# Performance work log

Measured on AMD Instinct MI355X. Metric: run time of the kernel, lower is better.

## Reference

```python
import jax, jax.numpy as jnp
import numpy as np

BATCH, SEQ = 2, 1024
D_MODEL, N_LAYER, VOCAB = 1024, 4, 32000
D_STATE, D_CONV, D_INNER, DT_RANK = 16, 4, 2048, 64  # expand=2, dt_rank=d_model//16
EPS = 1e-5


def setup_inputs() -> dict:
    key = jax.random.key(0)
    ks = jax.random.split(key, 8)
    s = 0.02
    tokens = jax.random.randint(ks[0], (BATCH, SEQ), 0, VOCAB)
    embed = jax.random.normal(ks[1], (VOCAB, D_MODEL), jnp.float32) * s
    norm_w = jnp.ones((N_LAYER, D_MODEL), jnp.float32)
    in_proj_w = jax.random.normal(ks[2], (N_LAYER, 2 * D_INNER, D_MODEL), jnp.float32) * s
    conv_w = jax.random.normal(ks[3], (N_LAYER, D_INNER, D_CONV), jnp.float32) * s
    conv_b = jnp.zeros((N_LAYER, D_INNER), jnp.float32)
    x_proj_w = jax.random.normal(ks[4], (N_LAYER, DT_RANK + 2 * D_STATE, D_INNER), jnp.float32) * s
    dt_w = jax.random.normal(ks[5], (N_LAYER, D_INNER, DT_RANK), jnp.float32) * s
    # softplus-inverse of 0.01 so initial dt is small and positive (mamba default style)
    dt_b = jnp.full((N_LAYER, D_INNER), float(np.log(np.expm1(0.01))), jnp.float32)
    # S4D-real init: A_n = n for n = 1..d_state
    A_log = jnp.log(jnp.broadcast_to(jnp.arange(1, D_STATE + 1, dtype=jnp.float32), (N_LAYER, D_INNER, D_STATE)))
    D_skip = jnp.ones((N_LAYER, D_INNER), jnp.float32)
    out_proj_w = jax.random.normal(ks[6], (N_LAYER, D_MODEL, D_INNER), jnp.float32) * s
    final_norm_w = jnp.ones((D_MODEL,), jnp.float32)
    return dict(tokens=tokens, embed=embed, norm_w=norm_w, in_proj_w=in_proj_w,
                conv_w=conv_w, conv_b=conv_b, x_proj_w=x_proj_w, dt_w=dt_w, dt_b=dt_b,
                A_log=A_log, D_skip=D_skip, out_proj_w=out_proj_w, final_norm_w=final_norm_w)


def rmsnorm(x, w):
    return x * jax.lax.rsqrt(jnp.mean(x * x, axis=-1, keepdims=True) + EPS) * w


def mamba_mixer(x, in_w, cw, cb, xp_w, dtw, dtb, A_log, Dsk, ow):
    # x: (B, L, D)
    xz = jnp.einsum('bld,ed->ble', x, in_w)          # (B, L, 2*d_inner)
    xi, z = jnp.split(xz, 2, axis=-1)
    # causal depthwise conv over L
    xt = jnp.pad(jnp.transpose(xi, (0, 2, 1)), ((0, 0), (0, 0), (D_CONV - 1, 0)))  # (B, C, L+pad)
    xc = jax.lax.conv_general_dilated(xt, cw[:, None, :], (1,), 'VALID',
                                      feature_group_count=D_INNER,
                                      dimension_numbers=('NCH', 'OIH', 'NCH'))
    xc = jax.nn.silu(jnp.transpose(xc, (0, 2, 1)) + cb)  # (B, L, C)
    # input-dependent dt, B, C
    x_dbl = jnp.einsum('blc,ec->ble', xc, xp_w)
    dtr = x_dbl[..., :DT_RANK]
    Bm = x_dbl[..., DT_RANK:DT_RANK + D_STATE]
    Cm = x_dbl[..., DT_RANK + D_STATE:]
    dt = jax.nn.softplus(jnp.einsum('blr,cr->blc', dtr, dtw) + dtb)  # (B, L, C)
    A = -jnp.exp(A_log)  # (C, S)

    def step(h, inp):
        dt_t, x_t, B_t, C_t = inp            # (B,C),(B,C),(B,S),(B,S)
        dA = jnp.exp(dt_t[..., None] * A)    # (B, C, S)
        h = dA * h + (dt_t * x_t)[..., None] * B_t[:, None, :]
        y = jnp.einsum('bcs,bs->bc', h, C_t)
        return h, y

    h0 = jnp.zeros((x.shape[0], D_INNER, D_STATE), x.dtype)
    xs = (jnp.moveaxis(dt, 1, 0), jnp.moveaxis(xc, 1, 0),
          jnp.moveaxis(Bm, 1, 0), jnp.moveaxis(Cm, 1, 0))
    _, ys = jax.lax.scan(step, h0, xs)
    y = jnp.moveaxis(ys, 0, 1) + xc * Dsk
    y = y * jax.nn.silu(z)
    return jnp.einsum('blc,dc->bld', y, ow)


def reference(tokens, embed, norm_w, in_proj_w, conv_w, conv_b, x_proj_w, dt_w, dt_b,
              A_log, D_skip, out_proj_w, final_norm_w):
    h = embed[tokens]  # (B, L, D)
    for i in range(N_LAYER):
        h = h + mamba_mixer(rmsnorm(h, norm_w[i]), in_proj_w[i], conv_w[i], conv_b[i],
                            x_proj_w[i], dt_w[i], dt_b[i], A_log[i], D_skip[i], out_proj_w[i])
    h = rmsnorm(h, final_norm_w)
    logits = jnp.einsum('bld,vd->blv', h, embed)  # tied lm_head
    return logits
```

## Files before the change

kernel.cpp:

```cpp
#include <hip/hip_runtime.h>
#include <cstdint>
#include <cstddef>

#define B_  2
#define L_  1024
#define DM  1024
#define DI  2048
#define DSN 16
#define DR  64

typedef short          s16x8 __attribute__((ext_vector_type(8)));
typedef float          f32x4 __attribute__((ext_vector_type(4)));
typedef unsigned short u16;
typedef unsigned short u16x4 __attribute__((ext_vector_type(4)));
typedef unsigned int   u32x4 __attribute__((ext_vector_type(4)));

__device__ __forceinline__ u16 f2bf(float f) {
  union { float f; unsigned int u; } v; v.f = f;
  unsigned int u = v.u;
  u += 0x7fffu + ((u >> 16) & 1u);
  return (u16)(u >> 16);
}

template <int CTRL>
__device__ __forceinline__ float dpp_add(float x) {
  union { float f; int i; } u, r;
  u.f = x;
  r.i = __builtin_amdgcn_update_dpp(0, u.i, CTRL, 0xf, 0xf, false);
  return x + r.f;
}

#define GLDS(gsrc, ldst)                                                      \
  __builtin_amdgcn_global_load_lds(                                           \
      (const __attribute__((address_space(1))) unsigned int*)(gsrc),          \
      (__attribute__((address_space(3))) unsigned int*)(ldst), 16, 0, 0)

__global__ __launch_bounds__(256) void k_cvt_bf16(const float* __restrict__ in,
                                                  u16* __restrict__ out, int n4) {
  int i = blockIdx.x * 256 + threadIdx.x;
  if (i < n4) {
    f32x4 v = *(const f32x4*)(in + (size_t)i * 4);
    u16x4 o;
    o[0] = f2bf(v[0]); o[1] = f2bf(v[1]); o[2] = f2bf(v[2]); o[3] = f2bf(v[3]);
    *(u16x4*)(out + (size_t)i * 4) = o;
  }
}

__global__ __launch_bounds__(256) void k_gather(const int* __restrict__ tok,
                                                const float* __restrict__ emb,
                                                float* __restrict__ h) {
  int row = blockIdx.x;
  int t = tok[row];
  f32x4 v = ((const f32x4*)(emb + (size_t)t * DM))[threadIdx.x];
  ((f32x4*)(h + (size_t)row * DM))[threadIdx.x] = v;
}

__global__ __launch_bounds__(256) void k_rmsnorm_bf16(const float* __restrict__ x,
                                                      const float* __restrict__ w,
                                                      u16* __restrict__ out) {
  int row = blockIdx.x;
  int tid = threadIdx.x;
  f32x4 v = ((const f32x4*)(x + (size_t)row * DM))[tid];
  float ss = v[0]*v[0] + v[1]*v[1] + v[2]*v[2] + v[3]*v[3];
  #pragma unroll
  for (int m = 1; m < 64; m <<= 1) ss += __shfl_xor(ss, m);
  __shared__ float red[4];
  if ((tid & 63) == 0) red[tid >> 6] = ss;
  __syncthreads();
  float tot = red[0] + red[1] + red[2] + red[3];
  float sc = rsqrtf(tot * (1.0f / DM) + 1e-5f);
  f32x4 wv = ((const f32x4*)w)[tid];
  u16x4 o;
  o[0] = f2bf(v[0]*sc*wv[0]); o[1] = f2bf(v[1]*sc*wv[1]);
  o[2] = f2bf(v[2]*sc*wv[2]); o[3] = f2bf(v[3]*sc*wv[3]);
  ((u16x4*)(out + (size_t)row * DM))[tid] = o;
}

__global__ __launch_bounds__(256) void k_conv_silu(const float* __restrict__ xz,
                                                   const float* __restrict__ cw,
                                                   const float* __restrict__ cb,
                                                   float* __restrict__ xcf,
                                                   u16* __restrict__ xcbf) {
  int e = blockIdx.x * 256 + threadIdx.x;
  int c = e & (DI - 1);
  int row = e >> 11;
  int l = row & (L_ - 1);
  const float* base = xz + (size_t)row * (2 * DI) + c;
  float acc = cb[c];
  float w0 = cw[c*4+0], w1 = cw[c*4+1], w2 = cw[c*4+2], w3 = cw[c*4+3];
  if (l >= 3) acc += base[-3 * (2 * DI)] * w0;
  if (l >= 2) acc += base[-2 * (2 * DI)] * w1;
  if (l >= 1) acc += base[-1 * (2 * DI)] * w2;
  acc += base[0] * w3;
  float s = acc / (1.f + __expf(-acc));
  xcf[e] = s;
  xcbf[e] = f2bf(s);
}

__global__ __launch_bounds__(256) void k_scan(const float* __restrict__ dt,
                                              const float* __restrict__ xcf,
                                              const float* __restrict__ xdbl,
                                              const float* __restrict__ xz,
                                              const float* __restrict__ A_log,
                                              const float* __restrict__ Dsk,
                                              u16* __restrict__ ybf) {
  const int b  = blockIdx.x >> 7;
  const int c0 = (blockIdx.x & 127) << 4;
  const int tid = threadIdx.x;
  const int cl = tid >> 4, s = tid & 15;
  const int c  = c0 + cl;
  const float a2  = -__expf(A_log[c * DSN + s]) * 1.4426950408889634f;
  const float dsk = Dsk[c];

  __shared__ __align__(16) float sdt[16][68], sxc[16][68], sB[16][68], sC[16][68];
  __shared__ float szg[64][17];

  float hs = 0.f, ysel = 0.f;
  const size_t rowbase = (size_t)b * L_;

  float gdt[4], gxc[4], gz[4], gB[4], gC[4];
  auto stage_load = [&](int t0) {
    #pragma unroll
    for (int k = 0; k < 4; ++k) {
      size_t r = rowbase + t0 + cl + 16 * k;
      gdt[k] = dt  [r * DI + c0 + s];
      gxc[k] = xcf [r * DI + c0 + s];
      gz[k]  = xz  [r * (2 * DI) + DI + c0 + s];
      gB[k]  = xdbl[r * 96 + 64 + s];
      gC[k]  = xdbl[r * 96 + 80 + s];
    }
  };
  auto stage_write = [&]() {
    #pragma unroll
    for (int k = 0; k < 4; ++k) {
      int tt = cl + 16 * k;
      sdt[s][tt] = gdt[k];
      sxc[s][tt] = gxc[k];
      sB [s][tt] = gB[k];
      sC [s][tt] = gC[k];
      szg[tt][s] = gz[k];
    }
  };

  stage_load(0);
  stage_write();
  __syncthreads();

  for (int t0 = 0; t0 < L_; t0 += 64) {
    const bool more = (t0 + 64) < L_;
    if (more) stage_load(t0 + 64);

    f32x4 vdt = *(const f32x4*)&sdt[cl][0];
    f32x4 vxc = *(const f32x4*)&sxc[cl][0];
    f32x4 vB  = *(const f32x4*)&sB [s][0];
    f32x4 vC  = *(const f32x4*)&sC [s][0];
    #pragma unroll
    for (int q = 0; q < 16; ++q) {
      f32x4 ndt, nxc, nB, nC;
      if (q < 15) {
        ndt = *(const f32x4*)&sdt[cl][q * 4 + 4];
        nxc = *(const f32x4*)&sxc[cl][q * 4 + 4];
        nB  = *(const f32x4*)&sB [s][q * 4 + 4];
        nC  = *(const f32x4*)&sC [s][q * 4 + 4];
      }
      #pragma unroll
      for (int j = 0; j < 4; ++j) {
        float dtvj = vdt[j], xvj = vxc[j];
        float dA = exp2f(dtvj * a2);
        hs = dA * hs + (dtvj * xvj) * vB[j];
        float yv = hs * vC[j];
        yv = dpp_add<0xB1>(yv);
        yv = dpp_add<0x4E>(yv);
        yv = dpp_add<0x141>(yv);
        yv = dpp_add<0x140>(yv);
        yv += xvj * dsk;
        const int sidx = ((q & 3) << 2) | j;
        ysel = (sidx == s) ? yv : ysel;
      }
      if ((q & 3) == 3) {
        int tt = ((q >> 2) << 4) + s;
        float zv = szg[tt][cl];
        float sig = __builtin_amdgcn_rcpf(1.f + __expf(-zv));
        float yo = ysel * (zv * sig);
        ybf[(rowbase + t0 + tt) * DI + c] = f2bf(yo);
      }
      if (q < 15) { vdt = ndt; vxc = nxc; vB = nB; vC = nC; }
    }
    __syncthreads();
    if (more) stage_write();
    __syncthreads();
  }
}

template <int WM, int WN, int EPI>
__global__ __launch_bounds__(256) void k_gemm(const u16* __restrict__ A,
                                              const u16* __restrict__ W,
                                              float* __restrict__ C,
                                              u16* __restrict__ aux,
                                              const float* __restrict__ bias,
                                              int M, int N, int K) {
  constexpr int BM = 32 * WM, BN = 32 * WN, BK = 32;
  __shared__ __align__(16) u16 As[BM * BK];
  __shared__ __align__(16) u16 Bs[BN * BK];
  const int tid = threadIdx.x;

  const int gx = gridDim.x;
  const int nwg = gx * gridDim.y;
  const int lin = blockIdx.y * gx + blockIdx.x;
  const int q8 = nwg >> 3, r8 = nwg & 7;
  const int xcd = lin & 7, loc = lin >> 3;
  const int swz = (xcd < r8 ? xcd * (q8 + 1) : r8 * (q8 + 1) + (xcd - r8) * q8) + loc;
  const int m0 = (swz / gx) * BM, n0 = (swz % gx) * BN;

  const int wave = tid >> 6, lane = tid & 63;
  const int wm = wave & 1, wn = wave >> 1;
  const int l15 = lane & 15, quad = lane >> 4;
  const int sr = lane >> 2, scc = lane & 3;

  f32x4 acc[WM][WN];
  #pragma unroll
  for (int i = 0; i < WM; ++i)
    #pragma unroll
    for (int j = 0; j < WN; ++j)
      acc[i][j] = f32x4{0.f, 0.f, 0.f, 0.f};

  constexpr int NA = BM / 16;
  constexpr int NB = BN / 16;

  for (int k0 = 0; k0 < K; k0 += BK) {
    for (int ch = wave; ch < NA; ch += 4) {
      int r = (ch << 4) + sr;
      GLDS(A + (size_t)(m0 + r) * K + k0 + (scc << 3), As + (ch << 9));
    }
    for (int ch = wave; ch < NB; ch += 4) {
      int r = (ch << 4) + sr;
      GLDS(W + (size_t)(n0 + r) * K + k0 + (scc << 3), Bs + (ch << 9));
    }
    __syncthreads();
    s16x8 af[WM], bfv[WN];
    #pragma unroll
    for (int i = 0; i < WM; ++i)
      af[i] = *(const s16x8*)(As + (wm * WM * 16 + i * 16 + l15) * BK + quad * 8);
    #pragma unroll
    for (int j = 0; j < WN; ++j)
      bfv[j] = *(const s16x8*)(Bs + (wn * WN * 16 + j * 16 + l15) * BK + quad * 8);
    #pragma unroll
    for (int i = 0; i < WM; ++i)
      #pragma unroll
      for (int j = 0; j < WN; ++j)
        acc[i][j] = __builtin_amdgcn_mfma_f32_16x16x32_bf16(af[i], bfv[j], acc[i][j], 0, 0, 0);
    __syncthreads();
  }

  #pragma unroll
  for (int i = 0; i < WM; ++i) {
    #pragma unroll
    for (int j = 0; j < WN; ++j) {
      int mb = m0 + wm * WM * 16 + i * 16 + quad * 4;
      int nb = n0 + wn * WN * 16 + j * 16 + l15;
      #pragma unroll
      for (int r = 0; r < 4; ++r) {
        size_t idx = (size_t)(mb + r) * N + nb;
        float v = acc[i][j][r];
        if constexpr (EPI == 1) v += C[idx];
        if constexpr (EPI == 2) {
          v += bias[nb];
          v = (v > 20.f) ? v : log1pf(__expf(v));
        }
        C[idx] = v;
        if constexpr (EPI == 3) {
          if (nb < DR) aux[(size_t)(mb + r) * DR + nb] = f2bf(v);
        }
      }
    }
  }
}

extern "C" void kernel_launch(void* const* d_in, const int* in_sizes, int n_in,
                              void* d_out, int out_size, void* d_ws, size_t ws_size,
                              hipStream_t stream) {
  const int*   tokens = (const int*)d_in[0];
  const float* embed  = (const float*)d_in[1];
  const float* norm_w = (const float*)d_in[2];
  const float* in_w   = (const float*)d_in[3];
  const float* conv_w = (const float*)d_in[4];
  const float* conv_b = (const float*)d_in[5];
  const float* xp_w   = (const float*)d_in[6];
  const float* dt_w   = (const float*)d_in[7];
  const float* dt_b   = (const float*)d_in[8];
  const float* A_log  = (const float*)d_in[9];
  const float* D_skip = (const float*)d_in[10];
  const float* out_w  = (const float*)d_in[11];
  const float* fnw    = (const float*)d_in[12];
  float* logits = (float*)d_out;

  char* ws = (char*)d_ws;
  size_t off = 0;
  auto alloc = [&](size_t bytes) -> void* {
    void* p = ws + off;
    off = (off + bytes + 255) & ~(size_t)255;
    return p;
  };
  const size_t R = (size_t)B_ * L_;
  float* h     = (float*)alloc(R * DM * 4);
  u16*   xbf   = (u16*)  alloc(R * DM * 2);
  float* xz    = (float*)alloc(R * 2 * DI * 4);
  float* xcf   = (float*)alloc(R * DI * 4);
  u16*   xcbf  = (u16*)  alloc(R * DI * 2);
  float* xdbl  = (float*)alloc(R * 96 * 4);
  u16*   dtrbf = (u16*)  alloc(R * DR * 2);
  float* dtv   = (float*)alloc(R * DI * 4);
  u16*   ybf   = (u16*)  alloc(R * DI * 2);
  u16*   w_in  = (u16*)  alloc((size_t)2 * DI * DM * 2);
  u16*   w_out = (u16*)  alloc((size_t)DM * DI * 2);
  u16*   w_xp  = (u16*)  alloc((size_t)96 * DI * 2);
  u16*   w_dt  = (u16*)  alloc((size_t)DI * DR * 2);
  u16*   embbf = (u16*)  alloc(32000ull * DM * 2);
  if (off > ws_size) return;

  auto cvt = [&](const float* src, u16* dst, size_t n) {
    int n4 = (int)(n / 4);
    k_cvt_bf16<<<(n4 + 255) / 256, 256, 0, stream>>>(src, dst, n4);
  };
  cvt(embed, embbf, 32000ull * DM);

  k_gather<<<(int)R, 256, 0, stream>>>(tokens, embed, h);

  for (int i = 0; i < 4; ++i) {
    cvt(in_w  + (size_t)i * 2 * DI * DM, w_in,  (size_t)2 * DI * DM);
    cvt(out_w + (size_t)i * DM * DI,     w_out, (size_t)DM * DI);
    cvt(xp_w  + (size_t)i * 96 * DI,     w_xp,  (size_t)96 * DI);
    cvt(dt_w  + (size_t)i * DI * DR,     w_dt,  (size_t)DI * DR);

    k_rmsnorm_bf16<<<(int)R, 256, 0, stream>>>(h, norm_w + i * DM, xbf);
    k_gemm<4, 4, 0><<<dim3(2 * DI / 128, (int)R / 128), 256, 0, stream>>>(
        xbf, w_in, xz, nullptr, nullptr, (int)R, 2 * DI, DM);
    k_conv_silu<<<(int)(R * DI) / 256, 256, 0, stream>>>(
        xz, conv_w + i * DI * 4, conv_b + i * DI, xcf, xcbf);
    k_gemm<2, 3, 3><<<dim3(1, (int)R / 64), 256, 0, stream>>>(
        xcbf, w_xp, xdbl, dtrbf, nullptr, (int)R, 96, DI);
    k_gemm<4, 4, 2><<<dim3(DI / 128, (int)R / 128), 256, 0, stream>>>(
        dtrbf, w_dt, dtv, nullptr, dt_b + i * DI, (int)R, DI, DR);
    k_scan<<<B_ * (DI / 16), 256, 0, stream>>>(
        dtv, xcf, xdbl, xz, A_log + i * DI * DSN, D_skip + i * DI, ybf);
    k_gemm<4, 4, 1><<<dim3(DM / 128, (int)R / 128), 256, 0, stream>>>(
        ybf, w_out, h, nullptr, nullptr, (int)R, DM, DI);
  }
  k_rmsnorm_bf16<<<(int)R, 256, 0, stream>>>(h, fnw, xbf);
  k_gemm<4, 4, 0><<<dim3(32000 / 128, (int)R / 128), 256, 0, stream>>>(
      xbf, embbf, logits, nullptr, nullptr, (int)R, 32000, DM);
}
```

Baseline: 1.656 ms.

## Split-K the x_proj GEMM, double-buffer scan LDS reads, reorder GEMM tile swizzle

The narrow x_proj GEMM (N=96, K=2048) previously ran on only 32 workgroups. It is now split 8 ways along K into partial buffers, followed by a new reduce kernel that sums the partials and writes both xdbl and the bf16 dt-rank slice. The scan's shared-memory operand prefetch goes two steps ahead instead of one, to hide LDS latency. The GEMM swizzle now walks M-fastest instead of N-fastest, which changes L2 reuse across XCDs. Costs are an extra launch and extra partial-sum memory traffic.

```diff
diff --git a/kernel.cpp b/kernel.cpp
--- a/kernel.cpp
+++ b/kernel.cpp
@@ -150,18 +150,20 @@
     const bool more = (t0 + 64) < L_;
     if (more) stage_load(t0 + 64);
 
-    f32x4 vdt = *(const f32x4*)&sdt[cl][0];
-    f32x4 vxc = *(const f32x4*)&sxc[cl][0];
-    f32x4 vB  = *(const f32x4*)&sB [s][0];
-    f32x4 vC  = *(const f32x4*)&sC [s][0];
+    f32x4 pdt[2], pxc[2], pB[2], pC[2];
+    pdt[0] = *(const f32x4*)&sdt[cl][0]; pdt[1] = *(const f32x4*)&sdt[cl][4];
+    pxc[0] = *(const f32x4*)&sxc[cl][0]; pxc[1] = *(const f32x4*)&sxc[cl][4];
+    pB[0]  = *(const f32x4*)&sB [s][0];  pB[1]  = *(const f32x4*)&sB [s][4];
+    pC[0]  = *(const f32x4*)&sC [s][0];  pC[1]  = *(const f32x4*)&sC [s][4];
     #pragma unroll
     for (int q = 0; q < 16; ++q) {
-      f32x4 ndt, nxc, nB, nC;
-      if (q < 15) {
-        ndt = *(const f32x4*)&sdt[cl][q * 4 + 4];
-        nxc = *(const f32x4*)&sxc[cl][q * 4 + 4];
-        nB  = *(const f32x4*)&sB [s][q * 4 + 4];
-        nC  = *(const f32x4*)&sC [s][q * 4 + 4];
+      const int cur = q & 1;
+      f32x4 vdt = pdt[cur], vxc = pxc[cur], vB = pB[cur], vC = pC[cur];
+      if (q < 14) {
+        pdt[cur] = *(const f32x4*)&sdt[cl][q * 4 + 8];
+        pxc[cur] = *(const f32x4*)&sxc[cl][q * 4 + 8];
+        pB[cur]  = *(const f32x4*)&sB [s][q * 4 + 8];
+        pC[cur]  = *(const f32x4*)&sC [s][q * 4 + 8];
       }
       #pragma unroll
       for (int j = 0; j < 4; ++j) {
@@ -184,7 +186,6 @@
         float yo = ysel * (zv * sig);
         ybf[(rowbase + t0 + tt) * DI + c] = f2bf(yo);
       }
-      if (q < 15) { vdt = ndt; vxc = nxc; vB = nB; vC = nC; }
     }
     __syncthreads();
     if (more) stage_write();
@@ -192,7 +193,7 @@
   }
 }
 
-template <int WM, int WN, int EPI>
+template <int WM, int WN, int EPI, int SK>
 __global__ __launch_bounds__(256) void k_gemm(const u16* __restrict__ A,
                                               const u16* __restrict__ W,
                                               float* __restrict__ C,
@@ -204,13 +205,21 @@
   __shared__ __align__(16) u16 Bs[BN * BK];
   const int tid = threadIdx.x;
 
-  const int gx = gridDim.x;
-  const int nwg = gx * gridDim.y;
-  const int lin = blockIdx.y * gx + blockIdx.x;
-  const int q8 = nwg >> 3, r8 = nwg & 7;
-  const int xcd = lin & 7, loc = lin >> 3;
-  const int swz = (xcd < r8 ? xcd * (q8 + 1) : r8 * (q8 + 1) + (xcd - r8) * q8) + loc;
-  const int m0 = (swz / gx) * BM, n0 = (swz % gx) * BN;
+  int m0, n0, kb = 0;
+  if constexpr (SK > 0) {
+    kb = blockIdx.x;
+    m0 = blockIdx.y * BM;
+    n0 = 0;
+  } else {
+    const int gx = gridDim.x, gy = gridDim.y;
+    const int nwg = gx * gy;
+    const int lin = blockIdx.y * gx + blockIdx.x;
+    const int q8 = nwg >> 3, r8 = nwg & 7;
+    const int xcd = lin & 7, loc = lin >> 3;
+    const int swz = (xcd < r8 ? xcd * (q8 + 1) : r8 * (q8 + 1) + (xcd - r8) * q8) + loc;
+    m0 = (swz % gy) * BM;
+    n0 = (swz / gy) * BN;
+  }
 
   const int wave = tid >> 6, lane = tid & 63;
   const int wm = wave & 1, wn = wave >> 1;
@@ -227,7 +236,10 @@
   constexpr int NA = BM / 16;
   constexpr int NB = BN / 16;
 
-  for (int k0 = 0; k0 < K; k0 += BK) {
+  const int kbeg = (SK > 0) ? kb * (K / (SK > 0 ? SK : 1)) : 0;
+  const int kend = (SK > 0) ? kbeg + K / (SK > 0 ? SK : 1) : K;
+
+  for (int k0 = kbeg; k0 < kend; k0 += BK) {
     for (int ch = wave; ch < NA; ch += 4) {
       int r = (ch << 4) + sr;
       GLDS(A + (size_t)(m0 + r) * K + k0 + (scc << 3), As + (ch << 9));
@@ -252,6 +264,7 @@
     __syncthreads();
   }
 
+  float* Cb = C + ((SK > 0) ? (size_t)kb * M * N : (size_t)0);
   #pragma unroll
   for (int i = 0; i < WM; ++i) {
     #pragma unroll
@@ -262,17 +275,36 @@
       for (int r = 0; r < 4; ++r) {
         size_t idx = (size_t)(mb + r) * N + nb;
         float v = acc[i][j][r];
-        if constexpr (EPI == 1) v += C[idx];
+        if constexpr (EPI == 1) v += Cb[idx];
         if constexpr (EPI == 2) {
           v += bias[nb];
           v = (v > 20.f) ? v : log1pf(__expf(v));
         }
-        C[idx] = v;
+        Cb[idx] = v;
         if constexpr (EPI == 3) {
           if (nb < DR) aux[(size_t)(mb + r) * DR + nb] = f2bf(v);
         }
       }
     }
+  }
+}
+
+__global__ __launch_bounds__(256) void k_xp_reduce(const float* __restrict__ part,
+                                                   float* __restrict__ xdbl,
+                                                   u16* __restrict__ dtr) {
+  int e = blockIdx.x * 256 + threadIdx.x;
+  int m = e / 24, n4 = e % 24;
+  f32x4 acc = *(const f32x4*)(part + (size_t)m * 96 + n4 * 4);
+  #pragma unroll
+  for (int kb = 1; kb < 8; ++kb) {
+    f32x4 p = *(const f32x4*)(part + (size_t)kb * (B_ * L_ * 96) + (size_t)m * 96 + n4 * 4);
+    acc[0] += p[0]; acc[1] += p[1]; acc[2] += p[2]; acc[3] += p[3];
+  }
+  *(f32x4*)(xdbl + (size_t)m * 96 + n4 * 4) = acc;
+  if (n4 < 16) {
+    u16x4 o;
+    o[0] = f2bf(acc[0]); o[1] = f2bf(acc[1]); o[2] = f2bf(acc[2]); o[3] = f2bf(acc[3]);
+    *(u16x4*)(dtr + (size_t)m * DR + n4 * 4) = o;
   }
 }
 
@@ -316,6 +348,7 @@
   u16*   w_xp  = (u16*)  alloc((size_t)96 * DI * 2);
   u16*   w_dt  = (u16*)  alloc((size_t)DI * DR * 2);
   u16*   embbf = (u16*)  alloc(32000ull * DM * 2);
+  float* xp_part = (float*)alloc((size_t)8 * R * 96 * 4);
   if (off > ws_size) return;
 
   auto cvt = [&](const float* src, u16* dst, size_t n) {
@@ -333,20 +366,21 @@
     cvt(dt_w  + (size_t)i * DI * DR,     w_dt,  (size_t)DI * DR);
 
     k_rmsnorm_bf16<<<(int)R, 256, 0, stream>>>(h, norm_w + i * DM, xbf);
-    k_gemm<4, 4, 0><<<dim3(2 * DI / 128, (int)R / 128), 256, 0, stream>>>(
+    k_gemm<4, 4, 0, 0><<<dim3(2 * DI / 128, (int)R / 128), 256, 0, stream>>>(
         xbf, w_in, xz, nullptr, nullptr, (int)R, 2 * DI, DM);
     k_conv_silu<<<(int)(R * DI) / 256, 256, 0, stream>>>(
         xz, conv_w + i * DI * 4, conv_b + i * DI, xcf, xcbf);
-    k_gemm<2, 3, 3><<<dim3(1, (int)R / 64), 256, 0, stream>>>(
-        xcbf, w_xp, xdbl, dtrbf, nullptr, (int)R, 96, DI);
-    k_gemm<4, 4, 2><<<dim3(DI / 128, (int)R / 128), 256, 0, stream>>>(
+    k_gemm<2, 3, 0, 8><<<dim3(8, (int)R / 64), 256, 0, stream>>>(
+        xcbf, w_xp, xp_part, nullptr, nullptr, (int)R, 96, DI);
+    k_xp_reduce<<<(int)(R * 24) / 256, 256, 0, stream>>>(xp_part, xdbl, dtrbf);
+    k_gemm<4, 4, 2, 0><<<dim3(DI / 128, (int)R / 128), 256, 0, stream>>>(
         dtrbf, w_dt, dtv, nullptr, dt_b + i * DI, (int)R, DI, DR);
     k_scan<<<B_ * (DI / 16), 256, 0, stream>>>(
         dtv, xcf, xdbl, xz, A_log + i * DI * DSN, D_skip + i * DI, ybf);
-    k_gemm<4, 4, 1><<<dim3(DM / 128, (int)R / 128), 256, 0, stream>>>(
+    k_gemm<4, 4, 1, 0><<<dim3(DM / 128, (int)R / 128), 256, 0, stream>>>(
         ybf, w_out, h, nullptr, nullptr, (int)R, DM, DI);
   }
   k_rmsnorm_bf16<<<(int)R, 256, 0, stream>>>(h, fnw, xbf);
-  k_gemm<4, 4, 0><<<dim3(32000 / 128, (int)R / 128), 256, 0, stream>>>(
+  k_gemm<4, 4, 0, 0><<<dim3(32000 / 128, (int)R / 128), 256, 0, stream>>>(
       xbf, embbf, logits, nullptr, nullptr, (int)R, 32000, DM);
 }
```

New measurement: 1.452 ms. 12.3% less time.
